# Kernel optimization log

Measured on AMD Instinct MI355X. Metric: run time of the kernel, lower is better.

## Reference

```python
import jax, jax.numpy as jnp
import numpy as np

N_NODES = 100000
IN_CH = 128
OUT_CH = 128
N_EDGES = 625000


def setup_inputs() -> dict:
    key = jax.random.key(0)
    k1, k2, k3, k4 = jax.random.split(key, 4)
    x = jax.random.normal(k1, (N_NODES, IN_CH), dtype=jnp.float32)
    edge_index = jax.random.randint(k2, (2, N_EDGES), 0, N_NODES, dtype=jnp.int64)
    # nn.Linear params (kaiming-uniform-ish init not needed for correctness; use scaled normal)
    W = jax.random.normal(k3, (OUT_CH, IN_CH), dtype=jnp.float32) / np.sqrt(IN_CH)
    b = jax.random.normal(k4, (OUT_CH,), dtype=jnp.float32) * 0.01
    return {"x": x, "edge_index": edge_index, "W": W, "b": b}


def reference(x, edge_index, W, b):
    # Linear: [N, in] @ [in, out] + [out]
    x_transformed = jnp.einsum("ni,oi->no", x, W) + b  # [N, out]
    src = edge_index[0]  # [E]
    dst = edge_index[1]  # [E]
    # scatter-add: neighbor_features[dst] += x_transformed[src]
    neighbor_features = jax.ops.segment_sum(
        x_transformed[src], dst, num_segments=x.shape[0]
    )  # [N, out]
    return neighbor_features + x_transformed
```

## Files before the change

### kernel.cpp

```cpp
#include <hip/hip_runtime.h>

constexpr int NN = 100000;
constexpr int CH = 128;
constexpr int NE = 625000;
constexpr int GEMM_BLOCKS = (NN + 63) / 64;
constexpr int BUCKET_BLOCKS = 256;
constexpr int EDGES_PER_BLOCK = (NE + BUCKET_BLOCKS - 1) / BUCKET_BLOCKS;
constexpr int NB = 196;
constexpr int CAP = 4096;
constexpr int WCONV_BLOCKS = 16;

typedef __bf16 bf16x8 __attribute__((ext_vector_type(8)));
typedef __bf16 bf16x4 __attribute__((ext_vector_type(4)));
typedef float  f32x4  __attribute__((ext_vector_type(4)));

__device__ __forceinline__ float bflo(uint u) { return __uint_as_float(u << 16); }
__device__ __forceinline__ float bfhi(uint u) { return __uint_as_float(u & 0xffff0000u); }

__global__ __launch_bounds__(256) void prep_kernel(
    int* __restrict__ gcursor, const float* __restrict__ W, __bf16* __restrict__ Wb)
{
    if (blockIdx.x == 0) {
        gcursor[threadIdx.x] = threadIdx.x * CAP;
        return;
    }
    int i = (blockIdx.x - 1) * 256 + threadIdx.x;
    int ch = i >> 5;
    int k0 = (i & 31) * 4;
    float4 v = reinterpret_cast<const float4*>(W)[i];
    bf16x4 h = {(__bf16)v.x, (__bf16)v.y, (__bf16)v.z, (__bf16)v.w};
    *reinterpret_cast<bf16x4*>(&Wb[ch * 128 + (k0 ^ ((ch & 7) << 3))]) = h;
}

__global__ __launch_bounds__(256) void gemm_bucket_kernel(
    const float* __restrict__ x, const __bf16* __restrict__ Wb,
    const float* __restrict__ b, __bf16* __restrict__ xt,
    const int* __restrict__ ei, int* __restrict__ gcursor, int2* __restrict__ pairs)
{
    __shared__ __bf16 wlds[128 * 128];
    __shared__ int lhist[256];
    __shared__ int lbase[256];
    const int tid = threadIdx.x;

    if (blockIdx.x < BUCKET_BLOCKS) {
        const int e0 = blockIdx.x * EDGES_PER_BLOCK;
        const int myN = min(NE - e0, EDGES_PER_BLOCK);
        lhist[tid] = 0;
        __syncthreads();
        for (int i = tid; i < myN; i += 256) {
            int dst = ei[NE + e0 + i];
            atomicAdd(&lhist[dst >> 9], 1);
        }
        __syncthreads();
        {
            int c = lhist[tid];
            if (c) lbase[tid] = atomicAdd(&gcursor[tid], c);
            lhist[tid] = 0;
        }
        __syncthreads();
        for (int i = tid; i < myN; i += 256) {
            int src = ei[e0 + i];
            int dst = ei[NE + e0 + i];
            int bin = dst >> 9;
            int r = atomicAdd(&lhist[bin], 1);
            pairs[lbase[bin] + r] = make_int2(src, dst);
        }
        return;
    }

    const bf16x8* Wb8 = reinterpret_cast<const bf16x8*>(Wb);
    #pragma unroll
    for (int it = 0; it < 8; ++it)
        reinterpret_cast<bf16x8*>(wlds)[it * 256 + tid] = Wb8[it * 256 + tid];

    const int lane = tid & 63;
    const int lm = lane & 15;
    const int lk = lane >> 4;
    const int row = (blockIdx.x - BUCKET_BLOCKS) * 64 + (tid >> 6) * 16 + lm;
    const int rc  = row < NN ? row : NN - 1;

    const float* xrow = x + (size_t)rc * CH;
    bf16x8 bfrag[4];
    #pragma unroll
    for (int ks = 0; ks < 4; ++ks) {
        const float4* p = reinterpret_cast<const float4*>(xrow + ks * 32 + lk * 8);
        float4 u = p[0], v = p[1];
        bfrag[ks][0] = (__bf16)u.x; bfrag[ks][1] = (__bf16)u.y;
        bfrag[ks][2] = (__bf16)u.z; bfrag[ks][3] = (__bf16)u.w;
        bfrag[ks][4] = (__bf16)v.x; bfrag[ks][5] = (__bf16)v.y;
        bfrag[ks][6] = (__bf16)v.z; bfrag[ks][7] = (__bf16)v.w;
    }

    __syncthreads();

    const float4* B4 = reinterpret_cast<const float4*>(b);
    const int swz = (lm & 7) << 3;

    #pragma unroll
    for (int t = 0; t < 8; ++t) {
        const int ch = t * 16 + lm;
        float4 bv = B4[t * 4 + lk];
        f32x4 acc = {bv.x, bv.y, bv.z, bv.w};
        #pragma unroll
        for (int ks = 0; ks < 4; ++ks) {
            bf16x8 afrag = *reinterpret_cast<const bf16x8*>(
                &wlds[ch * 128 + ((ks * 32 + lk * 8) ^ swz)]);
            acc = __builtin_amdgcn_mfma_f32_16x16x32_bf16(afrag, bfrag[ks], acc, 0, 0, 0);
        }
        if (row < NN) {
            const int c0 = t * 16 + lk * 4;
            bf16x4 hv = {(__bf16)acc[0], (__bf16)acc[1], (__bf16)acc[2], (__bf16)acc[3]};
            *reinterpret_cast<bf16x4*>(&xt[(size_t)row * CH + c0]) = hv;
        }
    }
}

__global__ __launch_bounds__(256) void place2_kernel(
    const int* __restrict__ gcursor, const int2* __restrict__ pairs,
    int* __restrict__ srcs, int* __restrict__ offs)
{
    __shared__ int cntb[256];
    __shared__ int cnt512[512];
    __shared__ int pref[512];
    __shared__ int dense_base;
    const int tid = threadIdx.x;
    const int bkt = blockIdx.x;

    int c = gcursor[tid] - tid * CAP;
    cntb[tid] = c;
    __syncthreads();
    for (int off = 1; off < 256; off <<= 1) {
        int u = (tid >= off) ? cntb[tid - off] : 0;
        __syncthreads();
        cntb[tid] += u;
        __syncthreads();
    }
    if (tid == bkt) dense_base = cntb[tid] - c;
    if (bkt == 0 && tid == 255) offs[NN] = cntb[255];
    __syncthreads();

    const int n = gcursor[bkt] - bkt * CAP;
    const int2* P = pairs + (size_t)bkt * CAP;

    cnt512[tid] = 0; cnt512[tid + 256] = 0;
    __syncthreads();
    for (int i = tid; i < n; i += 256)
        atomicAdd(&cnt512[P[i].y & 511], 1);
    __syncthreads();

    int c0 = cnt512[2 * tid], c1 = cnt512[2 * tid + 1];
    int ps = c0 + c1;
    cntb[tid] = ps;
    __syncthreads();
    for (int off = 1; off < 256; off <<= 1) {
        int u = (tid >= off) ? cntb[tid - off] : 0;
        __syncthreads();
        cntb[tid] += u;
        __syncthreads();
    }
    int ex = cntb[tid] - ps;
    pref[2 * tid] = ex;
    pref[2 * tid + 1] = ex + c0;

    {
        int d0 = bkt * 512 + 2 * tid;
        if (d0 < NN)     offs[d0]     = dense_base + ex;
        if (d0 + 1 < NN) offs[d0 + 1] = dense_base + ex + c0;
    }
    __syncthreads();

    for (int i = tid; i < n; i += 256) {
        int2 p = P[i];
        int pos = atomicAdd(&pref[p.y & 511], 1);
        srcs[dense_base + pos] = p.x;
    }
}

__global__ __launch_bounds__(256) void gather_kernel(
    const uint2* __restrict__ xtu2,
    const int* __restrict__ offs, const int* __restrict__ srcs,
    float* __restrict__ out)
{
    const int wid = (blockIdx.x * 256 + threadIdx.x) >> 6;
    if (wid >= NN) return;
    const int lane = threadIdx.x & 63;
    const int half = lane >> 5;
    const int l32  = lane & 31;

    uint2 own = xtu2[(size_t)wid * 32 + l32];

    float4 acc = {0.f, 0.f, 0.f, 0.f};
    int beg = offs[wid];
    const int end = offs[wid + 1];

    while (beg < end) {
        const int n = min(end - beg, 64);
        const int myidx = (lane < n) ? srcs[beg + lane] : 0;
        int k = 0;
        for (; k + 3 < n; k += 4) {
            int s0 = __shfl(myidx, k + half);
            int s1 = __shfl(myidx, k + 2 + half);
            uint2 h0 = xtu2[(size_t)s0 * 32 + l32];
            uint2 h1 = xtu2[(size_t)s1 * 32 + l32];
            acc.x += bflo(h0.x); acc.y += bfhi(h0.x);
            acc.z += bflo(h0.y); acc.w += bfhi(h0.y);
            acc.x += bflo(h1.x); acc.y += bfhi(h1.x);
            acc.z += bflo(h1.y); acc.w += bfhi(h1.y);
        }
        for (; k < n; k += 2) {
            const int kk = k + half;
            int s0 = __shfl(myidx, kk < n ? kk : 0);
            uint2 h0 = xtu2[(size_t)s0 * 32 + l32];
            if (kk < n) {
                acc.x += bflo(h0.x); acc.y += bfhi(h0.x);
                acc.z += bflo(h0.y); acc.w += bfhi(h0.y);
            }
        }
        beg += n;
    }

    acc.x += __shfl_xor(acc.x, 32);
    acc.y += __shfl_xor(acc.y, 32);
    acc.z += __shfl_xor(acc.z, 32);
    acc.w += __shfl_xor(acc.w, 32);

    if (half == 0) {
        acc.x += bflo(own.x); acc.y += bfhi(own.x);
        acc.z += bflo(own.y); acc.w += bfhi(own.y);
        reinterpret_cast<float4*>(out)[(size_t)wid * 32 + l32] = acc;
    }
}

extern "C" void kernel_launch(void* const* d_in, const int* in_sizes, int n_in,
                              void* d_out, int out_size, void* d_ws, size_t ws_size,
                              hipStream_t stream) {
    const float* x  = (const float*)d_in[0];
    const int*   ei = (const int*)d_in[1];
    const float* W  = (const float*)d_in[2];
    const float* b  = (const float*)d_in[3];
    float* out = (float*)d_out;

    __bf16* xt     = (__bf16*)d_ws;
    int2*   pairs  = (int2*)(xt + (size_t)NN * CH);
    int*    srcs   = (int*)(pairs + (size_t)256 * CAP);
    int*    offs   = srcs + NE;
    int*    gcur   = offs + NN + 1;
    __bf16* Wb     = (__bf16*)(gcur + 256);

    prep_kernel<<<1 + WCONV_BLOCKS, 256, 0, stream>>>(gcur, W, Wb);
    gemm_bucket_kernel<<<BUCKET_BLOCKS + GEMM_BLOCKS, 256, 0, stream>>>(
        x, Wb, b, xt, ei, gcur, pairs);
    place2_kernel<<<NB, 256, 0, stream>>>(gcur, pairs, srcs, offs);
    gather_kernel<<<(NN * 64 + 255) / 256, 256, 0, stream>>>(
        (const uint2*)xt, offs, srcs, out);
}
```

Before: 85.29 us.

## Process two row tiles per GEMM wave, alias bucket LDS, widen gather loads

The GEMM blocks now handle 128 rows (32 per wave, two MFMA accumulators per W fragment), so each W LDS read is reused twice and half as many blocks reload W into LDS. The bucket histogram arrays are aliased into the W LDS buffer to cut static shared memory. The gather kernel switches to 16-byte loads with four quarter-wave groups each fetching a different neighbor row, followed by a two-step shuffle reduction. This raises memory-level parallelism per instruction but adds registers and a slightly longer reduction.

```diff
diff --git a/kernel.cpp b/kernel.cpp
--- a/kernel.cpp
+++ b/kernel.cpp
@@ -3,7 +3,7 @@
 constexpr int NN = 100000;
 constexpr int CH = 128;
 constexpr int NE = 625000;
-constexpr int GEMM_BLOCKS = (NN + 63) / 64;
+constexpr int GEMM_BLOCKS = (NN + 127) / 128;
 constexpr int BUCKET_BLOCKS = 256;
 constexpr int EDGES_PER_BLOCK = (NE + BUCKET_BLOCKS - 1) / BUCKET_BLOCKS;
 constexpr int NB = 196;
@@ -38,11 +38,11 @@
     const int* __restrict__ ei, int* __restrict__ gcursor, int2* __restrict__ pairs)
 {
     __shared__ __bf16 wlds[128 * 128];
-    __shared__ int lhist[256];
-    __shared__ int lbase[256];
     const int tid = threadIdx.x;
 
     if (blockIdx.x < BUCKET_BLOCKS) {
+        int* lhist = (int*)wlds;
+        int* lbase = lhist + 256;
         const int e0 = blockIdx.x * EDGES_PER_BLOCK;
         const int myN = min(NE - e0, EDGES_PER_BLOCK);
         lhist[tid] = 0;
@@ -76,19 +76,29 @@
     const int lane = tid & 63;
     const int lm = lane & 15;
     const int lk = lane >> 4;
-    const int row = (blockIdx.x - BUCKET_BLOCKS) * 64 + (tid >> 6) * 16 + lm;
-    const int rc  = row < NN ? row : NN - 1;
-
-    const float* xrow = x + (size_t)rc * CH;
-    bf16x8 bfrag[4];
+    const int row0 = (blockIdx.x - BUCKET_BLOCKS) * 128 + (tid >> 6) * 32;
+    const int rowA = row0 + lm;
+    const int rowB = row0 + 16 + lm;
+    const int ra = rowA < NN ? rowA : NN - 1;
+    const int rb = rowB < NN ? rowB : NN - 1;
+    const float* xrowA = x + (size_t)ra * CH;
+    const float* xrowB = x + (size_t)rb * CH;
+
+    bf16x8 bfragA[4], bfragB[4];
     #pragma unroll
     for (int ks = 0; ks < 4; ++ks) {
-        const float4* p = reinterpret_cast<const float4*>(xrow + ks * 32 + lk * 8);
-        float4 u = p[0], v = p[1];
-        bfrag[ks][0] = (__bf16)u.x; bfrag[ks][1] = (__bf16)u.y;
-        bfrag[ks][2] = (__bf16)u.z; bfrag[ks][3] = (__bf16)u.w;
-        bfrag[ks][4] = (__bf16)v.x; bfrag[ks][5] = (__bf16)v.y;
-        bfrag[ks][6] = (__bf16)v.z; bfrag[ks][7] = (__bf16)v.w;
+        const float4* pa = reinterpret_cast<const float4*>(xrowA + ks * 32 + lk * 8);
+        const float4* pb = reinterpret_cast<const float4*>(xrowB + ks * 32 + lk * 8);
+        float4 u = pa[0], v = pa[1];
+        bfragA[ks][0] = (__bf16)u.x; bfragA[ks][1] = (__bf16)u.y;
+        bfragA[ks][2] = (__bf16)u.z; bfragA[ks][3] = (__bf16)u.w;
+        bfragA[ks][4] = (__bf16)v.x; bfragA[ks][5] = (__bf16)v.y;
+        bfragA[ks][6] = (__bf16)v.z; bfragA[ks][7] = (__bf16)v.w;
+        u = pb[0]; v = pb[1];
+        bfragB[ks][0] = (__bf16)u.x; bfragB[ks][1] = (__bf16)u.y;
+        bfragB[ks][2] = (__bf16)u.z; bfragB[ks][3] = (__bf16)u.w;
+        bfragB[ks][4] = (__bf16)v.x; bfragB[ks][5] = (__bf16)v.y;
+        bfragB[ks][6] = (__bf16)v.z; bfragB[ks][7] = (__bf16)v.w;
     }
 
     __syncthreads();
@@ -100,17 +110,23 @@
     for (int t = 0; t < 8; ++t) {
         const int ch = t * 16 + lm;
         float4 bv = B4[t * 4 + lk];
-        f32x4 acc = {bv.x, bv.y, bv.z, bv.w};
+        f32x4 acc0 = {bv.x, bv.y, bv.z, bv.w};
+        f32x4 acc1 = acc0;
         #pragma unroll
         for (int ks = 0; ks < 4; ++ks) {
             bf16x8 afrag = *reinterpret_cast<const bf16x8*>(
                 &wlds[ch * 128 + ((ks * 32 + lk * 8) ^ swz)]);
-            acc = __builtin_amdgcn_mfma_f32_16x16x32_bf16(afrag, bfrag[ks], acc, 0, 0, 0);
-        }
-        if (row < NN) {
-            const int c0 = t * 16 + lk * 4;
-            bf16x4 hv = {(__bf16)acc[0], (__bf16)acc[1], (__bf16)acc[2], (__bf16)acc[3]};
-            *reinterpret_cast<bf16x4*>(&xt[(size_t)row * CH + c0]) = hv;
+            acc0 = __builtin_amdgcn_mfma_f32_16x16x32_bf16(afrag, bfragA[ks], acc0, 0, 0, 0);
+            acc1 = __builtin_amdgcn_mfma_f32_16x16x32_bf16(afrag, bfragB[ks], acc1, 0, 0, 0);
+        }
+        const int c0 = t * 16 + lk * 4;
+        if (rowA < NN) {
+            bf16x4 hv = {(__bf16)acc0[0], (__bf16)acc0[1], (__bf16)acc0[2], (__bf16)acc0[3]};
+            *reinterpret_cast<bf16x4*>(&xt[(size_t)rowA * CH + c0]) = hv;
+        }
+        if (rowB < NN) {
+            bf16x4 hv = {(__bf16)acc1[0], (__bf16)acc1[1], (__bf16)acc1[2], (__bf16)acc1[3]};
+            *reinterpret_cast<bf16x4*>(&xt[(size_t)rowB * CH + c0]) = hv;
         }
     }
 }
@@ -177,19 +193,22 @@
 }
 
 __global__ __launch_bounds__(256) void gather_kernel(
-    const uint2* __restrict__ xtu2,
+    const uint4* __restrict__ xtu4,
     const int* __restrict__ offs, const int* __restrict__ srcs,
     float* __restrict__ out)
 {
     const int wid = (blockIdx.x * 256 + threadIdx.x) >> 6;
     if (wid >= NN) return;
     const int lane = threadIdx.x & 63;
-    const int half = lane >> 5;
-    const int l32  = lane & 31;
-
-    uint2 own = xtu2[(size_t)wid * 32 + l32];
-
-    float4 acc = {0.f, 0.f, 0.f, 0.f};
+    const int q   = lane >> 4;
+    const int l16 = lane & 15;
+
+    uint4 own = make_uint4(0u, 0u, 0u, 0u);
+    if (q == 0) own = xtu4[(size_t)wid * 16 + l16];
+
+    float a0 = 0.f, a1 = 0.f, a2 = 0.f, a3 = 0.f,
+          a4 = 0.f, a5 = 0.f, a6 = 0.f, a7 = 0.f;
+
     int beg = offs[wid];
     const int end = offs[wid + 1];
 
@@ -198,36 +217,44 @@
         const int myidx = (lane < n) ? srcs[beg + lane] : 0;
         int k = 0;
         for (; k + 3 < n; k += 4) {
-            int s0 = __shfl(myidx, k + half);
-            int s1 = __shfl(myidx, k + 2 + half);
-            uint2 h0 = xtu2[(size_t)s0 * 32 + l32];
-            uint2 h1 = xtu2[(size_t)s1 * 32 + l32];
-            acc.x += bflo(h0.x); acc.y += bfhi(h0.x);
-            acc.z += bflo(h0.y); acc.w += bfhi(h0.y);
-            acc.x += bflo(h1.x); acc.y += bfhi(h1.x);
-            acc.z += bflo(h1.y); acc.w += bfhi(h1.y);
-        }
-        for (; k < n; k += 2) {
-            const int kk = k + half;
-            int s0 = __shfl(myidx, kk < n ? kk : 0);
-            uint2 h0 = xtu2[(size_t)s0 * 32 + l32];
+            int s = __shfl(myidx, k + q);
+            uint4 h = xtu4[(size_t)s * 16 + l16];
+            a0 += bflo(h.x); a1 += bfhi(h.x);
+            a2 += bflo(h.y); a3 += bfhi(h.y);
+            a4 += bflo(h.z); a5 += bfhi(h.z);
+            a6 += bflo(h.w); a7 += bfhi(h.w);
+        }
+        if (k < n) {
+            const int kk = k + q;
+            int s = __shfl(myidx, kk < n ? kk : 0);
+            uint4 h = xtu4[(size_t)s * 16 + l16];
             if (kk < n) {
-                acc.x += bflo(h0.x); acc.y += bfhi(h0.x);
-                acc.z += bflo(h0.y); acc.w += bfhi(h0.y);
+                a0 += bflo(h.x); a1 += bfhi(h.x);
+                a2 += bflo(h.y); a3 += bfhi(h.y);
+                a4 += bflo(h.z); a5 += bfhi(h.z);
+                a6 += bflo(h.w); a7 += bfhi(h.w);
             }
         }
         beg += n;
     }
 
-    acc.x += __shfl_xor(acc.x, 32);
-    acc.y += __shfl_xor(acc.y, 32);
-    acc.z += __shfl_xor(acc.z, 32);
-    acc.w += __shfl_xor(acc.w, 32);
-
-    if (half == 0) {
-        acc.x += bflo(own.x); acc.y += bfhi(own.x);
-        acc.z += bflo(own.y); acc.w += bfhi(own.y);
-        reinterpret_cast<float4*>(out)[(size_t)wid * 32 + l32] = acc;
+    a0 += __shfl_xor(a0, 16); a0 += __shfl_xor(a0, 32);
+    a1 += __shfl_xor(a1, 16); a1 += __shfl_xor(a1, 32);
+    a2 += __shfl_xor(a2, 16); a2 += __shfl_xor(a2, 32);
+    a3 += __shfl_xor(a3, 16); a3 += __shfl_xor(a3, 32);
+    a4 += __shfl_xor(a4, 16); a4 += __shfl_xor(a4, 32);
+    a5 += __shfl_xor(a5, 16); a5 += __shfl_xor(a5, 32);
+    a6 += __shfl_xor(a6, 16); a6 += __shfl_xor(a6, 32);
+    a7 += __shfl_xor(a7, 16); a7 += __shfl_xor(a7, 32);
+
+    if (q == 0) {
+        a0 += bflo(own.x); a1 += bfhi(own.x);
+        a2 += bflo(own.y); a3 += bfhi(own.y);
+        a4 += bflo(own.z); a5 += bfhi(own.z);
+        a6 += bflo(own.w); a7 += bfhi(own.w);
+        float4* o4 = reinterpret_cast<float4*>(out) + (size_t)wid * 32 + l16 * 2;
+        o4[0] = make_float4(a0, a1, a2, a3);
+        o4[1] = make_float4(a4, a5, a6, a7);
     }
 }
 
@@ -252,5 +279,5 @@
         x, Wb, b, xt, ei, gcur, pairs);
     place2_kernel<<<NB, 256, 0, stream>>>(gcur, pairs, srcs, offs);
     gather_kernel<<<(NN * 64 + 255) / 256, 256, 0, stream>>>(
-        (const uint2*)xt, offs, srcs, out);
-}
+        (const uint4*)xt, offs, srcs, out);
+}
```

Result: no change. 86.11 us (+1.0%).

## Gather four nodes per wavefront with 16-byte loads, alias bucket LDS

Applied to the files above, without the earlier changes.

The gather kernel now gives each 16-lane group of a wavefront its own destination node. Each lane loads 16 bytes (8 bf16) per neighbor, so a wavefront handles four nodes instead of one and the cross-half shuffle reduction goes away. This cuts the wave count by four and widens the memory transactions for the random row gathers, at the cost of divergence when the four nodes have different degrees. Separately, the bucket histogram arrays reuse the GEMM weight LDS buffer, which reduces the kernel's static shared memory.

```diff
diff --git a/kernel.cpp b/kernel.cpp
--- a/kernel.cpp
+++ b/kernel.cpp
@@ -38,11 +38,11 @@
     const int* __restrict__ ei, int* __restrict__ gcursor, int2* __restrict__ pairs)
 {
     __shared__ __bf16 wlds[128 * 128];
-    __shared__ int lhist[256];
-    __shared__ int lbase[256];
     const int tid = threadIdx.x;
 
     if (blockIdx.x < BUCKET_BLOCKS) {
+        int* lhist = (int*)wlds;
+        int* lbase = lhist + 256;
         const int e0 = blockIdx.x * EDGES_PER_BLOCK;
         const int myN = min(NE - e0, EDGES_PER_BLOCK);
         lhist[tid] = 0;
@@ -177,57 +177,59 @@
 }
 
 __global__ __launch_bounds__(256) void gather_kernel(
-    const uint2* __restrict__ xtu2,
+    const uint4* __restrict__ xtu4,
     const int* __restrict__ offs, const int* __restrict__ srcs,
     float* __restrict__ out)
 {
-    const int wid = (blockIdx.x * 256 + threadIdx.x) >> 6;
-    if (wid >= NN) return;
+    const int gid  = blockIdx.x * 256 + threadIdx.x;
     const int lane = threadIdx.x & 63;
-    const int half = lane >> 5;
-    const int l32  = lane & 31;
-
-    uint2 own = xtu2[(size_t)wid * 32 + l32];
-
-    float4 acc = {0.f, 0.f, 0.f, 0.f};
-    int beg = offs[wid];
-    const int end = offs[wid + 1];
+    const int q    = lane >> 4;
+    const int l16  = lane & 15;
+    const int node = ((gid >> 6) << 2) + q;
+    const int nd   = node < NN ? node : NN - 1;
+
+    uint4 own = xtu4[(size_t)nd * 16 + l16];
+    float a0 = bflo(own.x), a1 = bfhi(own.x);
+    float a2 = bflo(own.y), a3 = bfhi(own.y);
+    float a4 = bflo(own.z), a5 = bfhi(own.z);
+    float a6 = bflo(own.w), a7 = bfhi(own.w);
+
+    int beg = offs[nd];
+    const int end = offs[nd + 1];
 
     while (beg < end) {
-        const int n = min(end - beg, 64);
-        const int myidx = (lane < n) ? srcs[beg + lane] : 0;
+        const int n = min(end - beg, 16);
+        const int myidx = (l16 < n) ? srcs[beg + l16] : 0;
         int k = 0;
-        for (; k + 3 < n; k += 4) {
-            int s0 = __shfl(myidx, k + half);
-            int s1 = __shfl(myidx, k + 2 + half);
-            uint2 h0 = xtu2[(size_t)s0 * 32 + l32];
-            uint2 h1 = xtu2[(size_t)s1 * 32 + l32];
-            acc.x += bflo(h0.x); acc.y += bfhi(h0.x);
-            acc.z += bflo(h0.y); acc.w += bfhi(h0.y);
-            acc.x += bflo(h1.x); acc.y += bfhi(h1.x);
-            acc.z += bflo(h1.y); acc.w += bfhi(h1.y);
-        }
-        for (; k < n; k += 2) {
-            const int kk = k + half;
-            int s0 = __shfl(myidx, kk < n ? kk : 0);
-            uint2 h0 = xtu2[(size_t)s0 * 32 + l32];
-            if (kk < n) {
-                acc.x += bflo(h0.x); acc.y += bfhi(h0.x);
-                acc.z += bflo(h0.y); acc.w += bfhi(h0.y);
-            }
+        for (; k + 1 < n; k += 2) {
+            int s0 = __shfl(myidx, (q << 4) + k);
+            int s1 = __shfl(myidx, (q << 4) + k + 1);
+            uint4 h0 = xtu4[(size_t)s0 * 16 + l16];
+            uint4 h1 = xtu4[(size_t)s1 * 16 + l16];
+            a0 += bflo(h0.x); a1 += bfhi(h0.x);
+            a2 += bflo(h0.y); a3 += bfhi(h0.y);
+            a4 += bflo(h0.z); a5 += bfhi(h0.z);
+            a6 += bflo(h0.w); a7 += bfhi(h0.w);
+            a0 += bflo(h1.x); a1 += bfhi(h1.x);
+            a2 += bflo(h1.y); a3 += bfhi(h1.y);
+            a4 += bflo(h1.z); a5 += bfhi(h1.z);
+            a6 += bflo(h1.w); a7 += bfhi(h1.w);
+        }
+        if (k < n) {
+            int s0 = __shfl(myidx, (q << 4) + k);
+            uint4 h0 = xtu4[(size_t)s0 * 16 + l16];
+            a0 += bflo(h0.x); a1 += bfhi(h0.x);
+            a2 += bflo(h0.y); a3 += bfhi(h0.y);
+            a4 += bflo(h0.z); a5 += bfhi(h0.z);
+            a6 += bflo(h0.w); a7 += bfhi(h0.w);
         }
         beg += n;
     }
 
-    acc.x += __shfl_xor(acc.x, 32);
-    acc.y += __shfl_xor(acc.y, 32);
-    acc.z += __shfl_xor(acc.z, 32);
-    acc.w += __shfl_xor(acc.w, 32);
-
-    if (half == 0) {
-        acc.x += bflo(own.x); acc.y += bfhi(own.x);
-        acc.z += bflo(own.y); acc.w += bfhi(own.y);
-        reinterpret_cast<float4*>(out)[(size_t)wid * 32 + l32] = acc;
+    if (node < NN) {
+        float4* o4 = reinterpret_cast<float4*>(out) + (size_t)node * 32 + l16 * 2;
+        o4[0] = make_float4(a0, a1, a2, a3);
+        o4[1] = make_float4(a4, a5, a6, a7);
     }
 }
 
@@ -251,6 +253,7 @@
     gemm_bucket_kernel<<<BUCKET_BLOCKS + GEMM_BLOCKS, 256, 0, stream>>>(
         x, Wb, b, xt, ei, gcur, pairs);
     place2_kernel<<<NB, 256, 0, stream>>>(gcur, pairs, srcs, offs);
-    gather_kernel<<<(NN * 64 + 255) / 256, 256, 0, stream>>>(
-        (const uint2*)xt, offs, srcs, out);
-}
+    const int gwaves = (NN + 3) / 4;
+    gather_kernel<<<(gwaves * 64 + 255) / 256, 256, 0, stream>>>(
+        (const uint4*)xt, offs, srcs, out);
+}
```

New measurement: 82.52 us. 1.03x faster.
